# Kernel optimization log

Hardware: AMD Instinct MI355X
Metric: run time of the kernel (lower is better)

Reference implementation:

```python
import jax, jax.numpy as jnp
import numpy as np

B, NT, D, V = 16, 4096, 512, 2545  # batch, text len, text_dim, text_num_embeds


def setup_inputs() -> dict:
    key = jax.random.key(0)
    k_txt, k_len, k_emb = jax.random.split(key, 3)
    text = jax.random.randint(k_txt, (B, NT), 0, V, dtype=jnp.int64)
    # ragged valid lengths; pad tail with -1 (-> token 0 after +1 shift)
    lengths = jax.random.randint(k_len, (B,), 1, NT + 1, dtype=jnp.int64)
    pos = jnp.arange(NT, dtype=jnp.int64)
    text = jnp.where(pos[None, :] < lengths[:, None], text, -1)
    emb = jax.random.normal(k_emb, (V + 1, D), dtype=jnp.float32) * 0.02
    return {"text": text, "seq_len": 4096, "emb": emb}


def _forward(emb, text, seq_len):
    t = text + 1
    t = t[:, :seq_len]
    t = jnp.pad(t, ((0, 0), (0, seq_len - t.shape[1])))  # pad with 0
    pad_mask = t == 0                      # [b, s] True at padding
    x = emb[t]                             # [b, s, d] embedding lookup
    # --- average upsample by valid mask (vectorized replacement of the
    #     per-batch Python loop in average_upsample_text_by_mask) ---
    valid = ~pad_mask
    L = valid.sum(axis=1)                  # [b] valid token counts
    # stable argsort of ~valid puts valid positions first, in order
    order = jnp.argsort(~valid, axis=1, stable=True)        # [b, s]
    gathered = jnp.take_along_axis(x, order[:, :, None], axis=1)  # [b, s, d]
    Ls = jnp.maximum(L, 1)
    base = seq_len // Ls                   # [b]
    rem = seq_len % Ls                     # [b]
    # token j repeats base times for j < L-rem, base+1 times for j >= L-rem
    pos = jnp.arange(seq_len, dtype=L.dtype)                # [s]
    boundary = (Ls - rem) * base           # [b] first output pos of the +1 block
    j_lo = pos[None, :] // base[:, None]
    j_hi = (Ls - rem)[:, None] + (pos[None, :] - boundary[:, None]) // (base + 1)[:, None]
    j = jnp.where(pos[None, :] < boundary[:, None], j_lo, j_hi)  # [b, s]
    out = jnp.take_along_axis(gathered, j[:, :, None], axis=1)   # [b, s, d]
    out = jnp.where((L == 0)[:, None, None], jnp.zeros((), out.dtype), out)
    return out


def reference(text, seq_len, emb):
    return _forward(emb, text, seq_len)
```

## Files before the change

kernel.cpp:

```cpp
#include <hip/hip_runtime.h>
#include <hip/hip_bf16.h>

#define B_   16
#define NT_  4096
#define D_   512
#define CHUNK 256

__global__ __launch_bounds__(256) void compact_kernel(const int* __restrict__ text,
                                                      int* __restrict__ tok,
                                                      int* __restrict__ meta) {
    const int b = blockIdx.x >> 4;
    const int c = blockIdx.x & 15;
    const int t = threadIdx.x;
    const int lane = t & 63;
    const int wid  = t >> 6;
    const int* row = text + b * NT_;

    int pre = 0;
    for (int i = t; i < c * CHUNK; i += 256) pre += (row[i] >= 0) ? 1 : 0;
    #pragma unroll
    for (int off = 32; off > 0; off >>= 1) pre += __shfl_down(pre, off, 64);
    __shared__ int s_pre[4];
    if (lane == 0) s_pre[wid] = pre;
    __syncthreads();
    const int chunk_base = s_pre[0] + s_pre[1] + s_pre[2] + s_pre[3];

    const int v = row[c * CHUNK + t];
    const int pred = (v >= 0) ? 1 : 0;
    int x = pred;
    #pragma unroll
    for (int off = 1; off < 64; off <<= 1) {
        int y = __shfl_up(x, off, 64);
        if (lane >= off) x += y;
    }
    __shared__ int s_wsum[4];
    if (lane == 63) s_wsum[wid] = x;
    __syncthreads();
    int woff = 0;
    for (int w = 0; w < wid; ++w) woff += s_wsum[w];

    if (pred) tok[b * NT_ + chunk_base + woff + (x - pred)] = v + 1;

    if (c == 15 && t == 255) {
        const int L  = chunk_base + woff + x;
        const int Ls = (L > 0) ? L : 1;
        const int base = NT_ / Ls;
        const int rem  = NT_ % Ls;
        meta[b * 4 + 0] = L;
        meta[b * 4 + 1] = base;
        meta[b * 4 + 2] = rem;
        meta[b * 4 + 3] = (Ls - rem) * base;
    }
}

__global__ __launch_bounds__(256) void map_kernel(const int* __restrict__ tok,
                                                  const int* __restrict__ meta,
                                                  int* __restrict__ exp_tok) {
    const int pidx = blockIdx.x * 256 + threadIdx.x;
    const int b = pidx >> 12;
    const int p = pidx & (NT_ - 1);
    const int L = meta[b * 4 + 0];
    int token = -1;
    if (L > 0) {
        const int base     = meta[b * 4 + 1];
        const int rem      = meta[b * 4 + 2];
        const int boundary = meta[b * 4 + 3];
        const int j = (p < boundary) ? (p / base)
                                     : ((L - rem) + (p - boundary) / (base + 1));
        token = tok[b * NT_ + j];
    }
    exp_tok[pidx] = token;
}

__global__ __launch_bounds__(256) void expand_kernel(const float4* __restrict__ emb,
                                                     const int* __restrict__ exp_tok,
                                                     float4* __restrict__ out) {
    const int tid  = blockIdx.x * 256 + threadIdx.x;
    const int pidx = tid >> 7;
    const int d4   = tid & 127;
    const int tkn  = exp_tok[pidx];
    float4 v;
    if (tkn < 0) {
        v = make_float4(0.f, 0.f, 0.f, 0.f);
    } else {
        v = emb[(size_t)tkn * (D_ / 4) + d4];
    }
    out[tid] = v;
}

extern "C" void kernel_launch(void* const* d_in, const int* in_sizes, int n_in,
                              void* d_out, int out_size, void* d_ws, size_t ws_size,
                              hipStream_t stream) {
    const int*   text = (const int*)d_in[0];
    const float* emb  = (const float*)d_in[2];
    float*       out  = (float*)d_out;

    int* tok     = (int*)d_ws;
    int* meta    = tok + B_ * NT_;
    int* exp_tok = meta + B_ * 4;

    compact_kernel<<<B_ * 16, 256, 0, stream>>>(text, tok, meta);
    map_kernel<<<(B_ * NT_) / 256, 256, 0, stream>>>(tok, meta, exp_tok);
    expand_kernel<<<(B_ * NT_ * (D_ / 4)) / 256, 256, 0, stream>>>(
        (const float4*)emb, exp_tok, (float4*)out);
}
```

Measured before the change: 158.1 us.

## Fuse index mapping into expand kernel with per-block token cache and nontemporal stores

Removes the separate map kernel. Each expand block now computes the source token indices for its 16 output positions into shared memory, then writes 8 float4 per thread. Output stores use nontemporal hints so the 128MB output does not pollute the cache. This saves one launch and the round trip through the exp_tok buffer, at the cost of a block barrier and fewer, larger blocks.

```diff
diff --git a/kernel.cpp b/kernel.cpp
--- a/kernel.cpp
+++ b/kernel.cpp
@@ -1,10 +1,11 @@
 #include <hip/hip_runtime.h>
-#include <hip/hip_bf16.h>
 
 #define B_   16
 #define NT_  4096
 #define D_   512
 #define CHUNK 256
+
+typedef float f4 __attribute__((ext_vector_type(4)));
 
 __global__ __launch_bounds__(256) void compact_kernel(const int* __restrict__ text,
                                                       int* __restrict__ tok,
@@ -53,39 +54,46 @@
     }
 }
 
-__global__ __launch_bounds__(256) void map_kernel(const int* __restrict__ tok,
-                                                  const int* __restrict__ meta,
-                                                  int* __restrict__ exp_tok) {
-    const int pidx = blockIdx.x * 256 + threadIdx.x;
-    const int b = pidx >> 12;
-    const int p = pidx & (NT_ - 1);
-    const int L = meta[b * 4 + 0];
-    int token = -1;
-    if (L > 0) {
-        const int base     = meta[b * 4 + 1];
-        const int rem      = meta[b * 4 + 2];
-        const int boundary = meta[b * 4 + 3];
-        const int j = (p < boundary) ? (p / base)
-                                     : ((L - rem) + (p - boundary) / (base + 1));
-        token = tok[b * NT_ + j];
+__global__ __launch_bounds__(256) void expand_fused(const f4* __restrict__ emb,
+                                                    const int* __restrict__ tok,
+                                                    const int* __restrict__ meta,
+                                                    f4* __restrict__ out) {
+    const int t     = threadIdx.x;
+    const int pidx0 = blockIdx.x << 4;
+    const int b     = pidx0 >> 12;
+
+    __shared__ int s_tok[16];
+    if (t < 16) {
+        const int p = (pidx0 & (NT_ - 1)) + t;
+        const int L = meta[b * 4 + 0];
+        int tkn = -1;
+        if (L > 0) {
+            const int base     = meta[b * 4 + 1];
+            const int rem      = meta[b * 4 + 2];
+            const int boundary = meta[b * 4 + 3];
+            const int j = (p < boundary) ? (p / base)
+                                         : ((L - rem) + (p - boundary) / (base + 1));
+            tkn = tok[b * NT_ + j];
+        }
+        s_tok[t] = tkn;
     }
-    exp_tok[pidx] = token;
-}
+    __syncthreads();
 
-__global__ __launch_bounds__(256) void expand_kernel(const float4* __restrict__ emb,
-                                                     const int* __restrict__ exp_tok,
-                                                     float4* __restrict__ out) {
-    const int tid  = blockIdx.x * 256 + threadIdx.x;
-    const int pidx = tid >> 7;
-    const int d4   = tid & 127;
-    const int tkn  = exp_tok[pidx];
-    float4 v;
-    if (tkn < 0) {
-        v = make_float4(0.f, 0.f, 0.f, 0.f);
-    } else {
-        v = emb[(size_t)tkn * (D_ / 4) + d4];
+    const size_t obase = (size_t)pidx0 * (D_ / 4);
+    #pragma unroll
+    for (int k = 0; k < 8; ++k) {
+        const int f   = k * 256 + t;
+        const int pl  = f >> 7;
+        const int d4  = f & 127;
+        const int tkn = s_tok[pl];
+        f4 v;
+        if (tkn < 0) {
+            v = (f4){0.f, 0.f, 0.f, 0.f};
+        } else {
+            v = emb[(size_t)tkn * (D_ / 4) + d4];
+        }
+        __builtin_nontemporal_store(v, &out[obase + f]);
     }
-    out[tid] = v;
 }
 
 extern "C" void kernel_launch(void* const* d_in, const int* in_sizes, int n_in,
@@ -93,14 +101,12 @@
                               hipStream_t stream) {
     const int*   text = (const int*)d_in[0];
     const float* emb  = (const float*)d_in[2];
-    float*       out  = (float*)d_out;
+    f4*          out  = (f4*)d_out;
 
-    int* tok     = (int*)d_ws;
-    int* meta    = tok + B_ * NT_;
-    int* exp_tok = meta + B_ * 4;
+    int* tok  = (int*)d_ws;
+    int* meta = tok + B_ * NT_;
 
     compact_kernel<<<B_ * 16, 256, 0, stream>>>(text, tok, meta);
-    map_kernel<<<(B_ * NT_) / 256, 256, 0, stream>>>(tok, meta, exp_tok);
-    expand_kernel<<<(B_ * NT_ * (D_ / 4)) / 256, 256, 0, stream>>>(
-        (const float4*)emb, exp_tok, (float4*)out);
+    expand_fused<<<(B_ * NT_) / 16, 256, 0, stream>>>(
+        (const f4*)emb, tok, meta, out);
 }
```

After: 158.8 us. No clear change (+0.4%).
